# Kernel optimization log

Measured on AMD Instinct MI355X. Metric: run time of the kernel, lower is better.

The kernel has to match this reference:

```python
import jax, jax.numpy as jnp
import numpy as np

B, N, H = 32, 1024, 256
ALPHA = 0.2  # leaky relu slope
NEG_INF = -1e12


def setup_inputs() -> dict:
    key = jax.random.key(0)
    k1, k2, k3, k4, k5, k6 = jax.random.split(key, 6)
    inp = jax.random.normal(k1, (B, N, H), dtype=jnp.float32)
    A = (jax.random.uniform(k2, (B, N, N)) < 0.05).astype(jnp.float32)
    l = jnp.sort(jax.random.randint(k3, (B, 2), 0, N), axis=1)
    # xavier-uniform(gain=1.414) approximated; exact init values are irrelevant for correctness
    lim_w = 1.414 * np.sqrt(6.0 / (H + H))
    W_i = jax.random.uniform(k4, (H, H), minval=-lim_w, maxval=lim_w, dtype=jnp.float32)
    W_c = jax.random.uniform(k5, (H, H), minval=-lim_w, maxval=lim_w, dtype=jnp.float32)
    lim_a = 1.414 * np.sqrt(6.0 / (2 * H + 1))
    a = jax.random.uniform(k6, (2 * H, 1), minval=-lim_a, maxval=lim_a, dtype=jnp.float32)
    return {"inp": inp, "A": A, "l": l, "W_i": W_i, "W_c": W_c, "a": a}


def reference(inp, A, l, W_i, W_c, a):
    # eval mode: dropout is identity (training=False)
    n = inp.shape[1]
    h = inp.shape[2]
    Wh_i = jnp.einsum('bnh,he->bne', inp, W_i)
    Wh_c = jnp.einsum('bnh,he->bne', inp, W_c)
    # vectorized replacement of the per-batch Wh[index][i:j] = Wh_i[index][i:j] loop
    idx = jnp.arange(n)
    sel = (idx[None, :] >= l[:, 0:1]) & (idx[None, :] < l[:, 1:2])  # [B,N]
    Wh = jnp.where(sel[:, :, None], Wh_i, Wh_c)
    # additive attention scores
    Wh1 = Wh @ a[:h, :]  # [B,N,1]
    Wh2 = Wh @ a[h:, :]  # [B,N,1]
    A_ = A + jnp.eye(n, dtype=A.dtype)
    e = jax.nn.leaky_relu((Wh1 + jnp.swapaxes(Wh2, 1, 2)) * A_, ALPHA)
    att = jnp.where(A_ > 0, e, NEG_INF)
    att = jax.nn.softmax(att, axis=2)
    h_prime = jnp.einsum('bnm,bme->bne', att, Wh)
    return jax.nn.elu(h_prime)  # concat=True
```

## Files before the change

### kernel.cpp

```cpp
#include <hip/hip_runtime.h>
#include <hip/hip_bf16.h>
#include <stdint.h>

#define B_ 32
#define N_ 1024
#define H_ 256

typedef short bf16x8 __attribute__((ext_vector_type(8)));
typedef float floatx4 __attribute__((ext_vector_type(4)));

__device__ inline unsigned short f2bs(float x) {
    __hip_bfloat16 h = __float2bfloat16(x);
    return __builtin_bit_cast(unsigned short, h);
}

__global__ __launch_bounds__(256)
void k_uvec(const float* __restrict__ Wi, const float* __restrict__ Wc,
            const float* __restrict__ a, float* __restrict__ U) {
    int k = blockIdx.x;
    int t = threadIdx.x;
    float wi = Wi[k * H_ + t];
    float wc = Wc[k * H_ + t];
    float a1 = a[t], a2 = a[H_ + t];
    float p0 = wi * a1, p1 = wc * a1, p2 = wi * a2, p3 = wc * a2;
    for (int off = 32; off; off >>= 1) {
        p0 += __shfl_xor(p0, off);
        p1 += __shfl_xor(p1, off);
        p2 += __shfl_xor(p2, off);
        p3 += __shfl_xor(p3, off);
    }
    __shared__ float red[4][4];
    int w = t >> 6;
    if ((t & 63) == 0) { red[w][0] = p0; red[w][1] = p1; red[w][2] = p2; red[w][3] = p3; }
    __syncthreads();
    if (t == 0) {
        U[0 * H_ + k] = red[0][0] + red[1][0] + red[2][0] + red[3][0];
        U[1 * H_ + k] = red[0][1] + red[1][1] + red[2][1] + red[3][1];
        U[2 * H_ + k] = red[0][2] + red[1][2] + red[2][2] + red[3][2];
        U[3 * H_ + k] = red[0][3] + red[1][3] + red[2][3] + red[3][3];
    }
}

__global__ __launch_bounds__(256)
void k_prep(const float* __restrict__ Wi, const float* __restrict__ Wc,
            unsigned short* __restrict__ WtFi, unsigned short* __restrict__ WtFc) {
    __shared__ float tile[64][65];
    int mat = blockIdx.x >> 4;
    int tr = ((blockIdx.x >> 2) & 3) * 64;
    int tc = (blockIdx.x & 3) * 64;
    const float* W = mat ? Wc : Wi;
    unsigned short* WtF = mat ? WtFc : WtFi;
    int t = threadIdx.x;
    int rr = t >> 2, c4 = (t & 3) * 16;
    const float* src = W + (size_t)(tr + rr) * H_ + tc + c4;
#pragma unroll
    for (int j = 0; j < 4; ++j) {
        float4 v = *reinterpret_cast<const float4*>(src + j * 4);
        tile[rr][c4 + 4 * j + 0] = v.x;
        tile[rr][c4 + 4 * j + 1] = v.y;
        tile[rr][c4 + 4 * j + 2] = v.z;
        tile[rr][c4 + 4 * j + 3] = v.w;
    }
    __syncthreads();
#pragma unroll
    for (int h = 0; h < 2; ++h) {
        int s = h * 256 + t;
        int ksl = s >> 8;
        int cl  = (s >> 6) & 3;
        int ll  = s & 63;
        int m16v = ll & 15, quadv = ll >> 4;
        int nloc = cl * 16 + m16v;
        int kb = ksl * 32 + quadv * 8;
        unsigned int pk[4];
#pragma unroll
        for (int jj = 0; jj < 4; ++jj) {
            unsigned short lo = f2bs(tile[kb + 2 * jj][nloc]);
            unsigned short hi = f2bs(tile[kb + 2 * jj + 1][nloc]);
            pk[jj] = (unsigned int)lo | ((unsigned int)hi << 16);
        }
        int ksg = (tr >> 5) + ksl;
        int cg  = (tc >> 4) + cl;
        *reinterpret_cast<uint4*>(WtF + ((size_t)(ksg * 16 + cg) * 64 + ll) * 8) =
            *reinterpret_cast<uint4*>(pk);
    }
}

__global__ __launch_bounds__(256)
void k_wh12(const float* __restrict__ inp, const int* __restrict__ l,
            const float* __restrict__ U,
            float* __restrict__ Wh1, float* __restrict__ Wh2,
            unsigned short* __restrict__ inpb) {
    int w = threadIdx.x >> 6, lane = threadIdx.x & 63;
    int row = blockIdx.x * 4 + w;
    int b = row >> 10, n = row & (N_ - 1);
    int l0 = l[2 * b], l1 = l[2 * b + 1];
    bool sel = (n >= l0) && (n < l1);
    const float* u1 = U + (sel ? 0 : H_);
    const float* u2 = U + 2 * H_ + (sel ? 0 : H_);
    const float4 x  = *reinterpret_cast<const float4*>(inp + (size_t)row * H_ + lane * 4);
    const float4 c1 = *reinterpret_cast<const float4*>(u1 + lane * 4);
    const float4 c2 = *reinterpret_cast<const float4*>(u2 + lane * 4);
    unsigned int p0 = (unsigned int)f2bs(x.x) | ((unsigned int)f2bs(x.y) << 16);
    unsigned int p1 = (unsigned int)f2bs(x.z) | ((unsigned int)f2bs(x.w) << 16);
    uint2 pk = {p0, p1};
    *reinterpret_cast<uint2*>(inpb + (size_t)row * H_ + lane * 4) = pk;

    float d1 = x.x * c1.x + x.y * c1.y + x.z * c1.z + x.w * c1.w;
    float d2 = x.x * c2.x + x.y * c2.y + x.z * c2.z + x.w * c2.w;
    for (int off = 32; off; off >>= 1) {
        d1 += __shfl_xor(d1, off);
        d2 += __shfl_xor(d2, off);
    }
    if (lane == 0) { Wh1[row] = d1; Wh2[row] = d2; }
}

__global__ __launch_bounds__(256)
void k_gemm(const unsigned short* __restrict__ inpb, const int* __restrict__ l,
            const unsigned short* __restrict__ WtFi, const unsigned short* __restrict__ WtFc,
            unsigned short* __restrict__ WhF) {
    __shared__ unsigned short bbuf[2][4096];
    int blk = blockIdx.x;
    int b  = blk >> 5;
    int r0 = ((blk >> 1) & 15) * 64;
    int n0 = (blk & 1) * 128;
    int t = threadIdx.x;
    int w = t >> 6;
    int lane = t & 63;
    int quad = lane >> 4, m16 = lane & 15;
    int rowb = r0 + w * 16;

    int l0 = l[2 * b], l1 = l[2 * b + 1];
    bool allI = (l0 <= r0) && (r0 + 64 <= l1);
    bool allC = (l1 <= r0) || (l0 >= r0 + 64);
    int npass = (allI || allC) ? 1 : 2;

    const unsigned short* arow = inpb + ((size_t)(b * N_ + rowb + m16)) * H_ + quad * 8;
    unsigned short* fb = WhF + (size_t)b * (N_ * H_);
    int cb = n0 >> 4;

    int j0 = rowb + quad * 4;
    int ksO = j0 >> 5;
    int laneF = m16 + 16 * ((j0 & 31) >> 3);
    int jj0 = j0 & 7;

    for (int pass = 0; pass < npass; ++pass) {
        const unsigned short* WtF =
            (npass == 1) ? (allI ? WtFi : WtFc) : (pass == 0 ? WtFi : WtFc);
        const unsigned short* gbase = WtF + cb * 512;

        floatx4 acc[8];
#pragma unroll
        for (int c = 0; c < 8; ++c) acc[c] = (floatx4){0.f, 0.f, 0.f, 0.f};

        {
            uint4 v0 = *reinterpret_cast<const uint4*>(gbase + (size_t)t * 8);
            uint4 v1 = *reinterpret_cast<const uint4*>(gbase + (size_t)(256 + t) * 8);
            *reinterpret_cast<uint4*>(&bbuf[0][t * 8]) = v0;
            *reinterpret_cast<uint4*>(&bbuf[0][(256 + t) * 8]) = v1;
        }
        for (int ks = 0; ks < 8; ++ks) {
            __syncthreads();
            uint4 v0, v1;
            if (ks < 7) {
                v0 = *reinterpret_cast<const uint4*>(gbase + (size_t)(ks + 1) * 8192 + t * 8);
                v1 = *reinterpret_cast<const uint4*>(gbase + (size_t)(ks + 1) * 8192 + (256 + t) * 8);
            }
            bf16x8 af = *reinterpret_cast<const bf16x8*>(arow + ks * 32);
            const unsigned short* bptr = &bbuf[ks & 1][lane * 8];
#pragma unroll
            for (int c = 0; c < 8; ++c) {
                bf16x8 bfr = *reinterpret_cast<const bf16x8*>(bptr + c * 512);
                acc[c] = __builtin_amdgcn_mfma_f32_16x16x32_bf16(af, bfr, acc[c], 0, 0, 0);
            }
            if (ks < 7) {
                *reinterpret_cast<uint4*>(&bbuf[(ks + 1) & 1][t * 8]) = v0;
                *reinterpret_cast<uint4*>(&bbuf[(ks + 1) & 1][(256 + t) * 8]) = v1;
            }
        }
        __syncthreads();

#pragma unroll
        for (int c = 0; c < 8; ++c) {
            size_t base = ((size_t)((ksO * 16 + cb + c) * 64) + laneF) * 8 + jj0;
            if (npass == 1) {
                unsigned int lo = (unsigned int)f2bs(acc[c][0]) | ((unsigned int)f2bs(acc[c][1]) << 16);
                unsigned int hi = (unsigned int)f2bs(acc[c][2]) | ((unsigned int)f2bs(acc[c][3]) << 16);
                uint2 v = {lo, hi};
                *reinterpret_cast<uint2*>(fb + base) = v;
            } else {
                bool want[4]; bool all = true, none = true;
#pragma unroll
                for (int r = 0; r < 4; ++r) {
                    int j = j0 + r;
                    bool sel = (j >= l0) && (j < l1);
                    want[r] = (pass == 0) ? sel : !sel;
                    all = all && want[r]; none = none && !want[r];
                }
                if (all) {
                    unsigned int lo = (unsigned int)f2bs(acc[c][0]) | ((unsigned int)f2bs(acc[c][1]) << 16);
                    unsigned int hi = (unsigned int)f2bs(acc[c][2]) | ((unsigned int)f2bs(acc[c][3]) << 16);
                    uint2 v = {lo, hi};
                    *reinterpret_cast<uint2*>(fb + base) = v;
                } else if (!none) {
#pragma unroll
                    for (int r = 0; r < 4; ++r)
                        if (want[r]) fb[base + r] = f2bs(acc[c][r]);
                }
            }
        }
    }
}

__global__ __launch_bounds__(256)
void k_attn(const float* __restrict__ A, const float* __restrict__ Wh1,
            const float* __restrict__ Wh2, const unsigned short* __restrict__ WhF,
            float* __restrict__ out) {
    __shared__ unsigned short pfrag[32 * 520];
    __shared__ float scl[16];
    int t = threadIdx.x, w = t >> 6, lane = t & 63;
    int bi = blockIdx.x;
    int b = (bi & 7) + 8 * (bi >> 9);
    int tile = (bi >> 3) & 63;
    int rowbase = tile * 16;

    const float* Wh2b = Wh2 + b * N_;
    float4 w2v[4];
#pragma unroll
    for (int ch = 0; ch < 4; ++ch)
        w2v[ch] = *reinterpret_cast<const float4*>(Wh2b + ch * 256 + lane * 4);

    int ksl = lane >> 3;
    int q2 = (lane >> 1) & 3;
    int jj0 = (lane & 1) * 4;

#pragma unroll
    for (int q = 0; q < 4; ++q) {
        int m = w * 4 + q;
        int i = rowbase + m;
        float wh1 = Wh1[b * N_ + i];
        const float* Arow = A + ((size_t)(b * N_ + i)) * N_;
        float e[16];
        float lmax = -1e30f;
#pragma unroll
        for (int ch = 0; ch < 4; ++ch) {
            float4 av = *reinterpret_cast<const float4*>(Arow + ch * 256 + lane * 4);
            if ((i >> 2) == (ch * 64 + lane)) ((float*)&av)[i & 3] += 1.0f;
            float aa[4] = {av.x, av.y, av.z, av.w};
            float ww[4] = {w2v[ch].x, w2v[ch].y, w2v[ch].z, w2v[ch].w};
#pragma unroll
            for (int c = 0; c < 4; ++c) {
                float p = (wh1 + ww[c]) * aa[c];
                float lv = fmaxf(p, 0.2f * p);
                e[ch * 4 + c] = aa[c] > 0.f ? lv : -1e30f;
                lmax = fmaxf(lmax, e[ch * 4 + c]);
            }
        }
        for (int off = 32; off; off >>= 1) lmax = fmaxf(lmax, __shfl_xor(lmax, off));

        float lsum = 0.f;
        unsigned int pk[8];
#pragma unroll
        for (int h2 = 0; h2 < 8; ++h2) {
            float p0 = e[2 * h2]     > -1e29f ? __expf(e[2 * h2]     - lmax) : 0.f;
            float p1 = e[2 * h2 + 1] > -1e29f ? __expf(e[2 * h2 + 1] - lmax) : 0.f;
            lsum += p0 + p1;
            pk[h2] = (unsigned int)f2bs(p0) | ((unsigned int)f2bs(p1) << 16);
        }
        for (int off = 32; off; off >>= 1) lsum += __shfl_xor(lsum, off);
        if (lane == 0) scl[m] = 1.0f / lsum;

#pragma unroll
        for (int ch = 0; ch < 4; ++ch) {
            int ks = ch * 8 + ksl;
            uint2 v = {pk[2 * ch], pk[2 * ch + 1]};
            *reinterpret_cast<uint2*>(pfrag + ks * 520 + (m + 16 * q2) * 8 + jj0) = v;
        }
    }
    __syncthreads();

    const unsigned short* WB = WhF + (size_t)b * (N_ * H_);
    floatx4 acc[4];
#pragma unroll
    for (int cc = 0; cc < 4; ++cc) acc[cc] = (floatx4){0.f, 0.f, 0.f, 0.f};
#pragma unroll 2
    for (int ks = 0; ks < 32; ++ks) {
        bf16x8 af = *reinterpret_cast<const bf16x8*>(pfrag + ks * 520 + lane * 8);
#pragma unroll
        for (int cc = 0; cc < 4; ++cc) {
            int c = w * 4 + cc;
            bf16x8 bfv = *reinterpret_cast<const bf16x8*>(
                WB + ((size_t)((ks * 16 + c) * 64 + lane)) * 8);
            acc[cc] = __builtin_amdgcn_mfma_f32_16x16x32_bf16(af, bfv, acc[cc], 0, 0, 0);
        }
    }

    int quad = lane >> 4, m16 = lane & 15;
#pragma unroll
    for (int cc = 0; cc < 4; ++cc) {
        int col = (w * 4 + cc) * 16 + m16;
#pragma unroll
        for (int r = 0; r < 4; ++r) {
            int m = quad * 4 + r;
            float v = acc[cc][r] * scl[m];
            v = v > 0.f ? v : __expf(v) - 1.0f;
            out[((size_t)(b * N_ + rowbase + m)) * H_ + col] = v;
        }
    }
}

extern "C" void kernel_launch(void* const* d_in, const int* in_sizes, int n_in,
                              void* d_out, int out_size, void* d_ws, size_t ws_size,
                              hipStream_t stream) {
    const float* inp = (const float*)d_in[0];
    const float* A   = (const float*)d_in[1];
    const int*   l   = (const int*)d_in[2];
    const float* Wi  = (const float*)d_in[3];
    const float* Wc  = (const float*)d_in[4];
    const float* a   = (const float*)d_in[5];
    float* out = (float*)d_out;

    char* ws = (char*)d_ws;
    size_t off = 0;
    unsigned short* WhF  = (unsigned short*)(ws + off); off += (size_t)B_ * N_ * H_ * 2;
    unsigned short* inpb = (unsigned short*)(ws + off); off += (size_t)B_ * N_ * H_ * 2;
    float* Wh1 = (float*)(ws + off); off += (size_t)B_ * N_ * 4;
    float* Wh2 = (float*)(ws + off); off += (size_t)B_ * N_ * 4;
    float* U   = (float*)(ws + off); off += 4 * H_ * 4;
    unsigned short* WtFi = (unsigned short*)(ws + off); off += (size_t)H_ * H_ * 2;
    unsigned short* WtFc = (unsigned short*)(ws + off); off += (size_t)H_ * H_ * 2;

    k_uvec<<<H_, 256, 0, stream>>>(Wi, Wc, a, U);
    k_prep<<<32, 256, 0, stream>>>(Wi, Wc, WtFi, WtFc);
    k_wh12<<<(B_ * N_) / 4, 256, 0, stream>>>(inp, l, U, Wh1, Wh2, inpb);
    k_gemm<<<B_ * 16 * 2, 256, 0, stream>>>(inpb, l, WtFi, WtFc, WhF);
    k_attn<<<B_ * (N_ / 16), 256, 0, stream>>>(A, Wh1, Wh2, WhF, out);
}
```

Before: 294.4 us.

## Fuse bf16 conversion and score projections into GEMM; double attention rows per block

Removes the separate k_wh12 pass: the GEMM kernel now reads fp32 inputs directly, converts them to bf16 in registers, and computes the Wh1/Wh2 dot products in the n0==0 blocks. This drops the bf16 inp intermediate buffer write/read and one launch. The attention kernel now handles 32 rows per block with two accumulator sets sharing each WhF B-fragment load, halving WhF reloads. In exchange, the fp32 input is re-read by both column-half blocks and across passes, and attention uses more LDS and registers with fewer blocks.

New measurement: 289.1 us. About the same (-1.8%).

```diff
diff --git a/kernel.cpp b/kernel.cpp
--- a/kernel.cpp
+++ b/kernel.cpp
@@ -86,38 +86,10 @@
 }
 
 __global__ __launch_bounds__(256)
-void k_wh12(const float* __restrict__ inp, const int* __restrict__ l,
-            const float* __restrict__ U,
-            float* __restrict__ Wh1, float* __restrict__ Wh2,
-            unsigned short* __restrict__ inpb) {
-    int w = threadIdx.x >> 6, lane = threadIdx.x & 63;
-    int row = blockIdx.x * 4 + w;
-    int b = row >> 10, n = row & (N_ - 1);
-    int l0 = l[2 * b], l1 = l[2 * b + 1];
-    bool sel = (n >= l0) && (n < l1);
-    const float* u1 = U + (sel ? 0 : H_);
-    const float* u2 = U + 2 * H_ + (sel ? 0 : H_);
-    const float4 x  = *reinterpret_cast<const float4*>(inp + (size_t)row * H_ + lane * 4);
-    const float4 c1 = *reinterpret_cast<const float4*>(u1 + lane * 4);
-    const float4 c2 = *reinterpret_cast<const float4*>(u2 + lane * 4);
-    unsigned int p0 = (unsigned int)f2bs(x.x) | ((unsigned int)f2bs(x.y) << 16);
-    unsigned int p1 = (unsigned int)f2bs(x.z) | ((unsigned int)f2bs(x.w) << 16);
-    uint2 pk = {p0, p1};
-    *reinterpret_cast<uint2*>(inpb + (size_t)row * H_ + lane * 4) = pk;
-
-    float d1 = x.x * c1.x + x.y * c1.y + x.z * c1.z + x.w * c1.w;
-    float d2 = x.x * c2.x + x.y * c2.y + x.z * c2.z + x.w * c2.w;
-    for (int off = 32; off; off >>= 1) {
-        d1 += __shfl_xor(d1, off);
-        d2 += __shfl_xor(d2, off);
-    }
-    if (lane == 0) { Wh1[row] = d1; Wh2[row] = d2; }
-}
-
-__global__ __launch_bounds__(256)
-void k_gemm(const unsigned short* __restrict__ inpb, const int* __restrict__ l,
+void k_gemm(const float* __restrict__ inp, const int* __restrict__ l,
             const unsigned short* __restrict__ WtFi, const unsigned short* __restrict__ WtFc,
-            unsigned short* __restrict__ WhF) {
+            unsigned short* __restrict__ WhF, const float* __restrict__ U,
+            float* __restrict__ Wh1, float* __restrict__ Wh2) {
     __shared__ unsigned short bbuf[2][4096];
     int blk = blockIdx.x;
     int b  = blk >> 5;
@@ -134,7 +106,14 @@
     bool allC = (l1 <= r0) || (l0 >= r0 + 64);
     int npass = (allI || allC) ? 1 : 2;
 
-    const unsigned short* arow = inpb + ((size_t)(b * N_ + rowb + m16)) * H_ + quad * 8;
+    int row = rowb + m16;
+    bool sel = (row >= l0) && (row < l1);
+    const float* xrow = inp + ((size_t)(b * N_ + row)) * H_;
+    const float* u1 = U + (sel ? 0 : H_);
+    const float* u2 = U + 2 * H_ + (sel ? 0 : H_);
+    bool doWh = (n0 == 0);
+    float d1 = 0.f, d2 = 0.f;
+
     unsigned short* fb = WhF + (size_t)b * (N_ * H_);
     int cb = n0 >> 4;
 
@@ -165,7 +144,25 @@
                 v0 = *reinterpret_cast<const uint4*>(gbase + (size_t)(ks + 1) * 8192 + t * 8);
                 v1 = *reinterpret_cast<const uint4*>(gbase + (size_t)(ks + 1) * 8192 + (256 + t) * 8);
             }
-            bf16x8 af = *reinterpret_cast<const bf16x8*>(arow + ks * 32);
+            const float4 xa = *reinterpret_cast<const float4*>(xrow + ks * 32 + quad * 8);
+            const float4 xb = *reinterpret_cast<const float4*>(xrow + ks * 32 + quad * 8 + 4);
+            if (pass == 0 && doWh) {
+                const float4 ua = *reinterpret_cast<const float4*>(u1 + ks * 32 + quad * 8);
+                const float4 ub = *reinterpret_cast<const float4*>(u1 + ks * 32 + quad * 8 + 4);
+                const float4 va = *reinterpret_cast<const float4*>(u2 + ks * 32 + quad * 8);
+                const float4 vb = *reinterpret_cast<const float4*>(u2 + ks * 32 + quad * 8 + 4);
+                d1 += xa.x * ua.x + xa.y * ua.y + xa.z * ua.z + xa.w * ua.w
+                    + xb.x * ub.x + xb.y * ub.y + xb.z * ub.z + xb.w * ub.w;
+                d2 += xa.x * va.x + xa.y * va.y + xa.z * va.z + xa.w * va.w
+                    + xb.x * vb.x + xb.y * vb.y + xb.z * vb.z + xb.w * vb.w;
+            }
+            unsigned int pk0 = (unsigned int)f2bs(xa.x) | ((unsigned int)f2bs(xa.y) << 16);
+            unsigned int pk1 = (unsigned int)f2bs(xa.z) | ((unsigned int)f2bs(xa.w) << 16);
+            unsigned int pk2 = (unsigned int)f2bs(xb.x) | ((unsigned int)f2bs(xb.y) << 16);
+            unsigned int pk3 = (unsigned int)f2bs(xb.z) | ((unsigned int)f2bs(xb.w) << 16);
+            uint4 apk = {pk0, pk1, pk2, pk3};
+            bf16x8 af = __builtin_bit_cast(bf16x8, apk);
+
             const unsigned short* bptr = &bbuf[ks & 1][lane * 8];
 #pragma unroll
             for (int c = 0; c < 8; ++c) {
@@ -192,8 +189,8 @@
 #pragma unroll
                 for (int r = 0; r < 4; ++r) {
                     int j = j0 + r;
-                    bool sel = (j >= l0) && (j < l1);
-                    want[r] = (pass == 0) ? sel : !sel;
+                    bool s2 = (j >= l0) && (j < l1);
+                    want[r] = (pass == 0) ? s2 : !s2;
                     all = all && want[r]; none = none && !want[r];
                 }
                 if (all) {
@@ -209,19 +206,28 @@
             }
         }
     }
+
+    if (doWh) {
+        d1 += __shfl_xor(d1, 16); d1 += __shfl_xor(d1, 32);
+        d2 += __shfl_xor(d2, 16); d2 += __shfl_xor(d2, 32);
+        if (quad == 0) {
+            Wh1[b * N_ + rowb + m16] = d1;
+            Wh2[b * N_ + rowb + m16] = d2;
+        }
+    }
 }
 
 __global__ __launch_bounds__(256)
 void k_attn(const float* __restrict__ A, const float* __restrict__ Wh1,
             const float* __restrict__ Wh2, const unsigned short* __restrict__ WhF,
             float* __restrict__ out) {
-    __shared__ unsigned short pfrag[32 * 520];
-    __shared__ float scl[16];
+    __shared__ unsigned short pfrag[2][32 * 520];
+    __shared__ float scl[32];
     int t = threadIdx.x, w = t >> 6, lane = t & 63;
     int bi = blockIdx.x;
-    int b = (bi & 7) + 8 * (bi >> 9);
-    int tile = (bi >> 3) & 63;
-    int rowbase = tile * 16;
+    int b = (bi & 7) * 4 + (bi >> 8);
+    int tile = (bi >> 3) & 31;
+    int rowbase = tile * 32;
 
     const float* Wh2b = Wh2 + b * N_;
     float4 w2v[4];
@@ -234,63 +240,71 @@
     int jj0 = (lane & 1) * 4;
 
 #pragma unroll
-    for (int q = 0; q < 4; ++q) {
-        int m = w * 4 + q;
-        int i = rowbase + m;
-        float wh1 = Wh1[b * N_ + i];
-        const float* Arow = A + ((size_t)(b * N_ + i)) * N_;
-        float e[16];
-        float lmax = -1e30f;
-#pragma unroll
-        for (int ch = 0; ch < 4; ++ch) {
-            float4 av = *reinterpret_cast<const float4*>(Arow + ch * 256 + lane * 4);
-            if ((i >> 2) == (ch * 64 + lane)) ((float*)&av)[i & 3] += 1.0f;
-            float aa[4] = {av.x, av.y, av.z, av.w};
-            float ww[4] = {w2v[ch].x, w2v[ch].y, w2v[ch].z, w2v[ch].w};
-#pragma unroll
-            for (int c = 0; c < 4; ++c) {
-                float p = (wh1 + ww[c]) * aa[c];
-                float lv = fmaxf(p, 0.2f * p);
-                e[ch * 4 + c] = aa[c] > 0.f ? lv : -1e30f;
-                lmax = fmaxf(lmax, e[ch * 4 + c]);
-            }
-        }
-        for (int off = 32; off; off >>= 1) lmax = fmaxf(lmax, __shfl_xor(lmax, off));
-
-        float lsum = 0.f;
-        unsigned int pk[8];
-#pragma unroll
-        for (int h2 = 0; h2 < 8; ++h2) {
-            float p0 = e[2 * h2]     > -1e29f ? __expf(e[2 * h2]     - lmax) : 0.f;
-            float p1 = e[2 * h2 + 1] > -1e29f ? __expf(e[2 * h2 + 1] - lmax) : 0.f;
-            lsum += p0 + p1;
-            pk[h2] = (unsigned int)f2bs(p0) | ((unsigned int)f2bs(p1) << 16);
-        }
-        for (int off = 32; off; off >>= 1) lsum += __shfl_xor(lsum, off);
-        if (lane == 0) scl[m] = 1.0f / lsum;
-
-#pragma unroll
-        for (int ch = 0; ch < 4; ++ch) {
-            int ks = ch * 8 + ksl;
-            uint2 v = {pk[2 * ch], pk[2 * ch + 1]};
-            *reinterpret_cast<uint2*>(pfrag + ks * 520 + (m + 16 * q2) * 8 + jj0) = v;
+    for (int tt = 0; tt < 2; ++tt) {
+#pragma unroll
+        for (int q = 0; q < 4; ++q) {
+            int m = w * 4 + q;
+            int i = rowbase + tt * 16 + m;
+            float wh1 = Wh1[b * N_ + i];
+            const float* Arow = A + ((size_t)(b * N_ + i)) * N_;
+            float e[16];
+            float lmax = -1e30f;
+#pragma unroll
+            for (int ch = 0; ch < 4; ++ch) {
+                float4 av = *reinterpret_cast<const float4*>(Arow + ch * 256 + lane * 4);
+                if ((i >> 2) == (ch * 64 + lane)) ((float*)&av)[i & 3] += 1.0f;
+                float aa[4] = {av.x, av.y, av.z, av.w};
+                float ww[4] = {w2v[ch].x, w2v[ch].y, w2v[ch].z, w2v[ch].w};
+#pragma unroll
+                for (int c = 0; c < 4; ++c) {
+                    float p = (wh1 + ww[c]) * aa[c];
+                    float lv = fmaxf(p, 0.2f * p);
+                    e[ch * 4 + c] = aa[c] > 0.f ? lv : -1e30f;
+                    lmax = fmaxf(lmax, e[ch * 4 + c]);
+                }
+            }
+            for (int off = 32; off; off >>= 1) lmax = fmaxf(lmax, __shfl_xor(lmax, off));
+
+            float lsum = 0.f;
+            unsigned int pk[8];
+#pragma unroll
+            for (int h2 = 0; h2 < 8; ++h2) {
+                float p0 = e[2 * h2]     > -1e29f ? __expf(e[2 * h2]     - lmax) : 0.f;
+                float p1 = e[2 * h2 + 1] > -1e29f ? __expf(e[2 * h2 + 1] - lmax) : 0.f;
+                lsum += p0 + p1;
+                pk[h2] = (unsigned int)f2bs(p0) | ((unsigned int)f2bs(p1) << 16);
+            }
+            for (int off = 32; off; off >>= 1) lsum += __shfl_xor(lsum, off);
+            if (lane == 0) scl[tt * 16 + m] = 1.0f / lsum;
+
+#pragma unroll
+            for (int ch = 0; ch < 4; ++ch) {
+                int ks = ch * 8 + ksl;
+                uint2 v = {pk[2 * ch], pk[2 * ch + 1]};
+                *reinterpret_cast<uint2*>(pfrag[tt] + ks * 520 + (m + 16 * q2) * 8 + jj0) = v;
+            }
         }
     }
     __syncthreads();
 
     const unsigned short* WB = WhF + (size_t)b * (N_ * H_);
-    floatx4 acc[4];
-#pragma unroll
-    for (int cc = 0; cc < 4; ++cc) acc[cc] = (floatx4){0.f, 0.f, 0.f, 0.f};
+    floatx4 acc0[4], acc1[4];
+#pragma unroll
+    for (int cc = 0; cc < 4; ++cc) {
+        acc0[cc] = (floatx4){0.f, 0.f, 0.f, 0.f};
+        acc1[cc] = (floatx4){0.f, 0.f, 0.f, 0.f};
+    }
 #pragma unroll 2
     for (int ks = 0; ks < 32; ++ks) {
-        bf16x8 af = *reinterpret_cast<const bf16x8*>(pfrag + ks * 520 + lane * 8);
+        bf16x8 af0 = *reinterpret_cast<const bf16x8*>(pfrag[0] + ks * 520 + lane * 8);
+        bf16x8 af1 = *reinterpret_cast<const bf16x8*>(pfrag[1] + ks * 520 + lane * 8);
 #pragma unroll
         for (int cc = 0; cc < 4; ++cc) {
             int c = w * 4 + cc;
             bf16x8 bfv = *reinterpret_cast<const bf16x8*>(
                 WB + ((size_t)((ks * 16 + c) * 64 + lane)) * 8);
-            acc[cc] = __builtin_amdgcn_mfma_f32_16x16x32_bf16(af, bfv, acc[cc], 0, 0, 0);
+            acc0[cc] = __builtin_amdgcn_mfma_f32_16x16x32_bf16(af0, bfv, acc0[cc], 0, 0, 0);
+            acc1[cc] = __builtin_amdgcn_mfma_f32_16x16x32_bf16(af1, bfv, acc1[cc], 0, 0, 0);
         }
     }
 
@@ -301,9 +315,12 @@
 #pragma unroll
         for (int r = 0; r < 4; ++r) {
             int m = quad * 4 + r;
-            float v = acc[cc][r] * scl[m];
-            v = v > 0.f ? v : __expf(v) - 1.0f;
-            out[((size_t)(b * N_ + rowbase + m)) * H_ + col] = v;
+            float v0 = acc0[cc][r] * scl[m];
+            v0 = v0 > 0.f ? v0 : __expf(v0) - 1.0f;
+            out[((size_t)(b * N_ + rowbase + m)) * H_ + col] = v0;
+            float v1 = acc1[cc][r] * scl[16 + m];
+            v1 = v1 > 0.f ? v1 : __expf(v1) - 1.0f;
+            out[((size_t)(b * N_ + rowbase + 16 + m)) * H_ + col] = v1;
         }
     }
 }
@@ -322,7 +339,6 @@
     char* ws = (char*)d_ws;
     size_t off = 0;
     unsigned short* WhF  = (unsigned short*)(ws + off); off += (size_t)B_ * N_ * H_ * 2;
-    unsigned short* inpb = (unsigned short*)(ws + off); off += (size_t)B_ * N_ * H_ * 2;
     float* Wh1 = (float*)(ws + off); off += (size_t)B_ * N_ * 4;
     float* Wh2 = (float*)(ws + off); off += (size_t)B_ * N_ * 4;
     float* U   = (float*)(ws + off); off += 4 * H_ * 4;
@@ -331,7 +347,6 @@
 
     k_uvec<<<H_, 256, 0, stream>>>(Wi, Wc, a, U);
     k_prep<<<32, 256, 0, stream>>>(Wi, Wc, WtFi, WtFc);
-    k_wh12<<<(B_ * N_) / 4, 256, 0, stream>>>(inp, l, U, Wh1, Wh2, inpb);
-    k_gemm<<<B_ * 16 * 2, 256, 0, stream>>>(inpb, l, WtFi, WtFc, WhF);
-    k_attn<<<B_ * (N_ / 16), 256, 0, stream>>>(A, Wh1, Wh2, WhF, out);
-}
+    k_gemm<<<B_ * 16 * 2, 256, 0, stream>>>(inp, l, WtFi, WtFc, WhF, U, Wh1, Wh2);
+    k_attn<<<B_ * (N_ / 32), 256, 0, stream>>>(A, Wh1, Wh2, WhF, out);
+}
```
